# Kernel tuning notes

Hardware: AMD Instinct MI355X
Metric: run time of the kernel (lower is better)

## Reference

```python
import jax, jax.numpy as jnp
import numpy as np

N, XDIM, D, K = 400000, 128, 3, 4
TWO_PI = 2.0 * np.pi


def _scaled(k, shape):
    fan_in = shape[0]
    return jax.random.normal(k, shape, jnp.float32) * np.float32(1.0 / np.sqrt(fan_in))


def setup_inputs() -> dict:
    key = jax.random.key(0)
    ks = jax.random.split(key, 9)
    return {
        "x1": jax.random.normal(ks[0], (N, XDIM), jnp.float32),
        "enc_w1": _scaled(ks[1], (XDIM, 16)), "enc_b1": jnp.zeros((16,), jnp.float32),
        "enc_w2": _scaled(ks[2], (16, 8)),   "enc_b2": jnp.zeros((8,), jnp.float32),
        "enc_w3": _scaled(ks[3], (8, 1)),    "enc_b3": jnp.zeros((1,), jnp.float32),
        "dec_w1": _scaled(ks[4], (1, 8)),    "dec_b1": jnp.zeros((8,), jnp.float32),
        "dec_w2": _scaled(ks[5], (8, 16)),   "dec_b2": jnp.zeros((16,), jnp.float32),
        "dec_w3": _scaled(ks[6], (16, XDIM)),"dec_b3": jnp.zeros((XDIM,), jnp.float32),
        "est_w1": _scaled(ks[7], (D, 8)),    "est_b1": jnp.zeros((8,), jnp.float32),
        "est_w2": _scaled(ks[8], (8, K)),    "est_b2": jnp.zeros((K,), jnp.float32),
    }


def reference(x1, enc_w1, enc_b1, enc_w2, enc_b2, enc_w3, enc_b3,
              dec_w1, dec_b1, dec_w2, dec_b2, dec_w3, dec_b3,
              est_w1, est_b1, est_w2, est_b2):
    # encoder: Dense(16,tanh)->Dense(8,tanh)->Dense(1,tanh)
    h = jnp.tanh(x1 @ enc_w1 + enc_b1)
    h = jnp.tanh(h @ enc_w2 + enc_b2)
    z1 = jnp.tanh(h @ enc_w3 + enc_b3)            # [N,1]
    # decoder: Dense(8,tanh)->Dense(16,tanh)->Dense(xdim, linear)
    h = jnp.tanh(z1 @ dec_w1 + dec_b1)
    h = jnp.tanh(h @ dec_w2 + dec_b2)
    x2 = h @ dec_w3 + dec_b3                      # [N,xdim]

    # relative distances
    dist_cos = jnp.sum(x1 * x2, axis=1, keepdims=True) / (
        jnp.linalg.norm(x1, axis=1, keepdims=True) * jnp.linalg.norm(x2, axis=1, keepdims=True))
    dist_euc = jnp.linalg.norm(x1 - x2, axis=1, keepdims=True)
    z = jnp.concatenate([z1, dist_cos, dist_euc], axis=1)   # [N,D]

    # estimator: Dense(8,tanh)->Dense(K,softmax)
    gamma = jax.nn.softmax(jnp.tanh(z @ est_w1 + est_b1) @ est_w2 + est_b2)  # [N,K]

    # GMM parameters from soft assignments
    gamma_sum = jnp.sum(gamma, axis=0)                        # [K]
    phi = jnp.mean(gamma, axis=0)                             # [K]
    mu = jnp.einsum('ik,il->kl', gamma, z) / gamma_sum[:, None]          # [K,D]
    z_centered = jnp.sqrt(gamma)[:, :, None] * (z[:, None, :] - mu[None, :, :])  # [N,K,D]
    sigma = jnp.einsum('ikl,ikm->klm', z_centered, z_centered) / gamma_sum[:, None, None]  # [K,D,D]

    # per-sample energy
    z_mu = z[:, None, :] - mu[None, :, :]                     # [N,K,D]
    sigma_inv = jnp.linalg.inv(sigma)                         # [K,D,D]
    item1 = jnp.log(phi)[None, :]                             # [1,K]
    item2 = -0.5 * jnp.einsum('nkd,kde,nke->nk', z_mu, sigma_inv, z_mu)  # [N,K]
    sigma_det = jnp.linalg.det(TWO_PI * sigma)                # [K]
    item3 = jnp.log(jnp.sqrt(sigma_det))[None, :]             # [1,K]
    energy = -jnp.sum(item1 + item2 - item3, axis=1)          # [N]

    # loss
    lambda1, lambda2 = 0.01, 0.0001
    diag = jnp.diagonal(sigma, axis1=-2, axis2=-1)            # [K,D]
    loss3 = lambda2 * jnp.sum(1.0 / diag)
    loss2 = lambda1 * jnp.mean(energy)
    loss1 = jnp.mean(jnp.sum(jnp.square(x1 - x2), axis=1))
    loss = loss1 + loss2 + loss3
    return energy, loss
```

## Files before the change

### kernel.cpp

```cpp
#include <hip/hip_runtime.h>

#define NSAMP 400000
#define NBLK  1563


__device__ __forceinline__ float ftanh(float x) {
    float e = __expf(2.0f * x);
    return 1.0f - __fdividef(2.0f, e + 1.0f);
}

__global__ __launch_bounds__(256) void prep_kernel(const float* __restrict__ dw3,
                                                   const float* __restrict__ db3,
                                                   float* __restrict__ Gm,
                                                   float* __restrict__ gv,
                                                   float* __restrict__ bb) {
    int t = threadIdx.x;
    int a = t >> 4, b = t & 15;
    float s = 0.f;
    for (int j = 0; j < 128; ++j) s += dw3[a * 128 + j] * dw3[b * 128 + j];
    Gm[t] = s;
    if (t < 16) {
        float sg = 0.f;
        for (int j = 0; j < 128; ++j) sg += dw3[t * 128 + j] * db3[j];
        gv[t] = sg;
    }
    if (t == 0) {
        float sbv = 0.f;
        for (int j = 0; j < 128; ++j) sbv += db3[j] * db3[j];
        *bb = sbv;
    }
}

__global__ __launch_bounds__(256) void pass1_kernel(
    const float* __restrict__ x1,
    const float* __restrict__ ew1, const float* __restrict__ eb1,
    const float* __restrict__ ew2, const float* __restrict__ eb2,
    const float* __restrict__ ew3, const float* __restrict__ eb3,
    const float* __restrict__ dw1, const float* __restrict__ db1,
    const float* __restrict__ dw2, const float* __restrict__ db2,
    const float* __restrict__ dw3, const float* __restrict__ db3,
    const float* __restrict__ tw1, const float* __restrict__ tb1,
    const float* __restrict__ tw2, const float* __restrict__ tb2,
    const float* __restrict__ Gm, const float* __restrict__ gv,
    const float* __restrict__ bbp,
    double* __restrict__ acc, float4* __restrict__ zbuf) {
    int i = blockIdx.x * 256 + threadIdx.x;
    bool active = (i < NSAMP);
    int row = active ? i : 0;
    const float4* xr = (const float4*)(x1 + (size_t)row * 128);

    float u[16], v[16];
#pragma unroll
    for (int k = 0; k < 16; ++k) { u[k] = 0.f; v[k] = 0.f; }
    float s2 = 0.f, sb = 0.f;

    float4 buf[4];
#pragma unroll
    for (int c = 0; c < 4; ++c) buf[c] = xr[c];

#pragma unroll 1
    for (int blk = 0; blk < 8; ++blk) {
        float xe[16];
#pragma unroll
        for (int c = 0; c < 4; ++c) {
            xe[c * 4 + 0] = buf[c].x; xe[c * 4 + 1] = buf[c].y;
            xe[c * 4 + 2] = buf[c].z; xe[c * 4 + 3] = buf[c].w;
        }
        if (blk < 7) {
#pragma unroll
            for (int c = 0; c < 4; ++c) buf[c] = xr[(blk + 1) * 4 + c];
        }
        int j0 = blk * 16;
#pragma unroll
        for (int e = 0; e < 16; ++e) {
            float x = xe[e];
            s2 = fmaf(x, x, s2);
            sb = fmaf(x, db3[j0 + e], sb);
#pragma unroll
            for (int k = 0; k < 16; ++k) u[k] = fmaf(x, ew1[(j0 + e) * 16 + k], u[k]);
        }
#pragma unroll
        for (int q = 0; q < 16; ++q) {
            float a2 = v[q];
#pragma unroll
            for (int e = 0; e < 16; ++e) a2 = fmaf(xe[e], dw3[q * 128 + j0 + e], a2);
            v[q] = a2;
        }
    }

    float h1[16];
#pragma unroll
    for (int k = 0; k < 16; ++k) h1[k] = ftanh(u[k] + eb1[k]);
    float h2[8];
#pragma unroll
    for (int m = 0; m < 8; ++m) {
        float a2 = eb2[m];
#pragma unroll
        for (int k = 0; k < 16; ++k) a2 = fmaf(h1[k], ew2[k * 8 + m], a2);
        h2[m] = ftanh(a2);
    }
    float a3 = eb3[0];
#pragma unroll
    for (int m = 0; m < 8; ++m) a3 = fmaf(h2[m], ew3[m], a3);
    float z1 = ftanh(a3);

    float d1[8];
#pragma unroll
    for (int p = 0; p < 8; ++p) d1[p] = ftanh(fmaf(z1, dw1[p], db1[p]));
    float d2[16];
#pragma unroll
    for (int q = 0; q < 16; ++q) {
        float a2 = db2[q];
#pragma unroll
        for (int p = 0; p < 8; ++p) a2 = fmaf(d1[p], dw2[p * 16 + q], a2);
        d2[q] = ftanh(a2);
    }

    float dot = sb;
#pragma unroll
    for (int q = 0; q < 16; ++q) dot = fmaf(d2[q], v[q], dot);
    float n2 = *bbp;
#pragma unroll
    for (int a = 0; a < 16; ++a) {
        float ra = 2.0f * gv[a];
#pragma unroll
        for (int b = 0; b < 16; ++b) ra = fmaf(Gm[a * 16 + b], d2[b], ra);
        n2 = fmaf(d2[a], ra, n2);
    }
    n2 = fmaxf(n2, 1e-20f);
    float euc2 = fmaxf(s2 - 2.0f * dot + n2, 0.f);
    float deuc = sqrtf(euc2);
    float dcos = dot * rsqrtf(s2 * n2);

    float zf[3] = {z1, dcos, deuc};

    float e1[8];
#pragma unroll
    for (int p = 0; p < 8; ++p) {
        float a2 = tb1[p];
        a2 = fmaf(zf[0], tw1[0 * 8 + p], a2);
        a2 = fmaf(zf[1], tw1[1 * 8 + p], a2);
        a2 = fmaf(zf[2], tw1[2 * 8 + p], a2);
        e1[p] = ftanh(a2);
    }
    float lg[4];
#pragma unroll
    for (int k = 0; k < 4; ++k) {
        float a2 = tb2[k];
#pragma unroll
        for (int p = 0; p < 8; ++p) a2 = fmaf(e1[p], tw2[p * 4 + k], a2);
        lg[k] = a2;
    }
    float mx = fmaxf(fmaxf(lg[0], lg[1]), fmaxf(lg[2], lg[3]));
    float ex[4]; float se = 0.f;
#pragma unroll
    for (int k = 0; k < 4; ++k) { ex[k] = __expf(lg[k] - mx); se += ex[k]; }
    float inv = __fdividef(1.0f, se);
    float gam[4];
#pragma unroll
    for (int k = 0; k < 4; ++k) gam[k] = ex[k] * inv;

    if (active) zbuf[i] = make_float4(zf[0], zf[1], zf[2], 0.f);
    if (!active) { gam[0] = gam[1] = gam[2] = gam[3] = 0.f; euc2 = 0.f; }

    __shared__ float sPart[4][41];
    int lane = threadIdx.x & 63;
    int wid = threadIdx.x >> 6;

#define REDUCE_STORE(T, VAL) { float _v = (VAL);                          \
        _v += __shfl_down(_v, 32); _v += __shfl_down(_v, 16);             \
        _v += __shfl_down(_v, 8);  _v += __shfl_down(_v, 4);              \
        _v += __shfl_down(_v, 2);  _v += __shfl_down(_v, 1);              \
        if (lane == 0) sPart[wid][T] = _v; }

#pragma unroll
    for (int k = 0; k < 4; ++k) REDUCE_STORE(k, gam[k]);
#pragma unroll
    for (int k = 0; k < 4; ++k) {
#pragma unroll
        for (int d = 0; d < 3; ++d) REDUCE_STORE(4 + k * 3 + d, gam[k] * zf[d]);
    }
#pragma unroll
    for (int k = 0; k < 4; ++k) {
        REDUCE_STORE(16 + k * 6 + 0, gam[k] * zf[0] * zf[0]);
        REDUCE_STORE(16 + k * 6 + 1, gam[k] * zf[0] * zf[1]);
        REDUCE_STORE(16 + k * 6 + 2, gam[k] * zf[0] * zf[2]);
        REDUCE_STORE(16 + k * 6 + 3, gam[k] * zf[1] * zf[1]);
        REDUCE_STORE(16 + k * 6 + 4, gam[k] * zf[1] * zf[2]);
        REDUCE_STORE(16 + k * 6 + 5, gam[k] * zf[2] * zf[2]);
    }
    REDUCE_STORE(40, euc2);
#undef REDUCE_STORE

    __syncthreads();
    if (threadIdx.x < 41) {
        double s = (double)sPart[0][threadIdx.x] + (double)sPart[1][threadIdx.x]
                 + (double)sPart[2][threadIdx.x] + (double)sPart[3][threadIdx.x];
        unsafeAtomicAdd(&acc[threadIdx.x], s);
    }
}

__global__ void gmm_kernel(double* __restrict__ acc, float* __restrict__ P) {
    if (threadIdx.x != 0 || blockIdx.x != 0) return;
    double M[6] = {0, 0, 0, 0, 0, 0}, bv[3] = {0, 0, 0}, A = 0.0, loss3 = 0.0;
    const double TWO_PI = 6.283185307179586;
    for (int k = 0; k < 4; ++k) {
        double g = acc[k];
        double phi = g / (double)NSAMP;
        double mu0 = acc[4 + k * 3 + 0] / g;
        double mu1 = acc[4 + k * 3 + 1] / g;
        double mu2 = acc[4 + k * 3 + 2] / g;
        double S00 = acc[16 + k * 6 + 0] / g - mu0 * mu0;
        double S01 = acc[16 + k * 6 + 1] / g - mu0 * mu1;
        double S02 = acc[16 + k * 6 + 2] / g - mu0 * mu2;
        double S11 = acc[16 + k * 6 + 3] / g - mu1 * mu1;
        double S12 = acc[16 + k * 6 + 4] / g - mu1 * mu2;
        double S22 = acc[16 + k * 6 + 5] / g - mu2 * mu2;
        double c00 = S11 * S22 - S12 * S12;
        double c01 = S02 * S12 - S01 * S22;
        double c02 = S01 * S12 - S02 * S11;
        double det = S00 * c00 + S01 * c01 + S02 * c02;
        double id = 1.0 / det;
        double I00 = c00 * id, I01 = c01 * id, I02 = c02 * id;
        double I11 = (S00 * S22 - S02 * S02) * id;
        double I12 = (S01 * S02 - S00 * S12) * id;
        double I22 = (S00 * S11 - S01 * S01) * id;
        M[0] += I00; M[1] += I01; M[2] += I02; M[3] += I11; M[4] += I12; M[5] += I22;
        double b0 = I00 * mu0 + I01 * mu1 + I02 * mu2;
        double b1 = I01 * mu0 + I11 * mu1 + I12 * mu2;
        double b2 = I02 * mu0 + I12 * mu1 + I22 * mu2;
        bv[0] += b0; bv[1] += b1; bv[2] += b2;
        double quad = mu0 * b0 + mu1 * b1 + mu2 * b2;
        A += -log(phi) + 0.5 * log(TWO_PI * TWO_PI * TWO_PI * det) + 0.5 * quad;
        loss3 += 1e-4 * (1.0 / S00 + 1.0 / S11 + 1.0 / S22);
    }
    P[0] = (float)M[0]; P[1] = (float)M[1]; P[2] = (float)M[2];
    P[3] = (float)M[3]; P[4] = (float)M[4]; P[5] = (float)M[5];
    P[6] = (float)bv[0]; P[7] = (float)bv[1]; P[8] = (float)bv[2];
    P[9] = (float)A;
    acc[42] = acc[40] / (double)NSAMP + loss3;
}

__global__ __launch_bounds__(256) void energy_kernel(const float4* __restrict__ zbuf,
                                                     const float* __restrict__ P,
                                                     double* __restrict__ acc,
                                                     float* __restrict__ out) {
    int i = blockIdx.x * 256 + threadIdx.x;
    float e = 0.f;
    if (i < NSAMP) {
        float4 z4 = zbuf[i];
        float z0 = z4.x, z1 = z4.y, z2 = z4.z;
        float q = P[0] * z0 * z0 + P[3] * z1 * z1 + P[5] * z2 * z2
                + 2.f * (P[1] * z0 * z1 + P[2] * z0 * z2 + P[4] * z1 * z2);
        e = P[9] + 0.5f * q - (P[6] * z0 + P[7] * z1 + P[8] * z2);
        out[i] = e;
    }
    float s = e;
    s += __shfl_down(s, 32); s += __shfl_down(s, 16); s += __shfl_down(s, 8);
    s += __shfl_down(s, 4);  s += __shfl_down(s, 2);  s += __shfl_down(s, 1);
    __shared__ float sE[4];
    if ((threadIdx.x & 63) == 0) sE[threadIdx.x >> 6] = s;
    __syncthreads();
    if (threadIdx.x == 0) {
        double t = (double)sE[0] + (double)sE[1] + (double)sE[2] + (double)sE[3];
        unsafeAtomicAdd(&acc[41], t);
    }
}

__global__ void final_kernel(const double* __restrict__ acc, float* __restrict__ out) {
    if (threadIdx.x == 0 && blockIdx.x == 0)
        out[NSAMP] = (float)(acc[42] + 0.01 * acc[41] / (double)NSAMP);
}

extern "C" void kernel_launch(void* const* d_in, const int* in_sizes, int n_in,
                              void* d_out, int out_size, void* d_ws, size_t ws_size,
                              hipStream_t stream) {
    const float* x1  = (const float*)d_in[0];
    const float* ew1 = (const float*)d_in[1];
    const float* eb1 = (const float*)d_in[2];
    const float* ew2 = (const float*)d_in[3];
    const float* eb2 = (const float*)d_in[4];
    const float* ew3 = (const float*)d_in[5];
    const float* eb3 = (const float*)d_in[6];
    const float* dw1 = (const float*)d_in[7];
    const float* db1 = (const float*)d_in[8];
    const float* dw2 = (const float*)d_in[9];
    const float* db2 = (const float*)d_in[10];
    const float* dw3 = (const float*)d_in[11];
    const float* db3 = (const float*)d_in[12];
    const float* tw1 = (const float*)d_in[13];
    const float* tb1 = (const float*)d_in[14];
    const float* tw2 = (const float*)d_in[15];
    const float* tb2 = (const float*)d_in[16];
    float* out = (float*)d_out;
    char* ws = (char*)d_ws;
    double* acc = (double*)ws;
    float* P    = (float*)(ws + 384);
    float* Gm   = (float*)(ws + 1024);
    float* gv   = (float*)(ws + 2048);
    float* bb   = (float*)(ws + 2112);
    float4* zb  = (float4*)(ws + 4096);

    hipMemsetAsync(d_ws, 0, 512, stream);
    prep_kernel<<<1, 256, 0, stream>>>(dw3, db3, Gm, gv, bb);
    pass1_kernel<<<NBLK, 256, 0, stream>>>(x1, ew1, eb1, ew2, eb2, ew3, eb3,
                                           dw1, db1, dw2, db2, dw3, db3,
                                           tw1, tb1, tw2, tb2, Gm, gv, bb, acc, zb);
    gmm_kernel<<<1, 64, 0, stream>>>(acc, P);
    energy_kernel<<<NBLK, 256, 0, stream>>>(zb, P, acc, out);
    final_kernel<<<1, 64, 0, stream>>>(acc, out);
}
```

Before: 455.5 us.

## Stage x1 tiles via global_load_lds with swizzle, fold final kernel into energy

The main pass now loads each 16-column slice of x1 for the whole block cooperatively, using global_load_lds into a swizzled LDS buffer. This gives coalesced global reads in place of each thread streaming its own 512-byte row, and each thread then reads its row back from LDS. The cost is two block barriers per slice and the loss of the old register prefetch, so the load of the next slice no longer overlaps with compute. The final scalar kernel is removed: the last energy block, found with an atomic counter, writes the loss. The prep kernel also caches dw3 and db3 in shared memory.

```diff
diff --git a/kernel.cpp b/kernel.cpp
--- a/kernel.cpp
+++ b/kernel.cpp
@@ -14,19 +14,24 @@
                                                    float* __restrict__ Gm,
                                                    float* __restrict__ gv,
                                                    float* __restrict__ bb) {
+    __shared__ float sw3[2048];
+    __shared__ float sb3[128];
     int t = threadIdx.x;
+    for (int k = t; k < 2048; k += 256) sw3[k] = dw3[k];
+    if (t < 128) sb3[t] = db3[t];
+    __syncthreads();
     int a = t >> 4, b = t & 15;
     float s = 0.f;
-    for (int j = 0; j < 128; ++j) s += dw3[a * 128 + j] * dw3[b * 128 + j];
+    for (int j = 0; j < 128; ++j) s = fmaf(sw3[a * 128 + j], sw3[b * 128 + j], s);
     Gm[t] = s;
     if (t < 16) {
         float sg = 0.f;
-        for (int j = 0; j < 128; ++j) sg += dw3[t * 128 + j] * db3[j];
+        for (int j = 0; j < 128; ++j) sg = fmaf(sw3[t * 128 + j], sb3[j], sg);
         gv[t] = sg;
     }
     if (t == 0) {
         float sbv = 0.f;
-        for (int j = 0; j < 128; ++j) sbv += db3[j] * db3[j];
+        for (int j = 0; j < 128; ++j) sbv = fmaf(sb3[j], sb3[j], sbv);
         *bb = sbv;
     }
 }
@@ -44,31 +49,45 @@
     const float* __restrict__ Gm, const float* __restrict__ gv,
     const float* __restrict__ bbp,
     double* __restrict__ acc, float4* __restrict__ zbuf) {
-    int i = blockIdx.x * 256 + threadIdx.x;
+    __shared__ float4 lbuf[1024];
+    __shared__ float sPart[4][41];
+
+    int t = threadIdx.x;
+    int i = blockIdx.x * 256 + t;
     bool active = (i < NSAMP);
-    int row = active ? i : 0;
-    const float4* xr = (const float4*)(x1 + (size_t)row * 128);
+    int bbase = blockIdx.x * 256;
+    int w = t >> 6, lane = t & 63;
+    int sw2 = (t >> 1) & 3;
+    const float4* x1f4 = (const float4*)x1;
 
     float u[16], v[16];
 #pragma unroll
     for (int k = 0; k < 16; ++k) { u[k] = 0.f; v[k] = 0.f; }
     float s2 = 0.f, sb = 0.f;
 
-    float4 buf[4];
-#pragma unroll
-    for (int c = 0; c < 4; ++c) buf[c] = xr[c];
-
 #pragma unroll 1
     for (int blk = 0; blk < 8; ++blk) {
+#pragma unroll
+        for (int c2 = 0; c2 < 4; ++c2) {
+            int idx = (w * 4 + c2) * 64 + lane;
+            int row = idx >> 2, qs = idx & 3;
+            int q = qs ^ ((row >> 1) & 3);
+            int grow = bbase + row;
+            if (grow >= NSAMP) grow = NSAMP - 1;
+            const float4* src = x1f4 + (size_t)grow * 32 + blk * 4 + q;
+            float4* dst = lbuf + (w * 4 + c2) * 64;
+            __builtin_amdgcn_global_load_lds(
+                (const __attribute__((address_space(1))) void*)src,
+                (__attribute__((address_space(3))) void*)dst, 16, 0, 0);
+        }
+        __syncthreads();
+
         float xe[16];
 #pragma unroll
-        for (int c = 0; c < 4; ++c) {
-            xe[c * 4 + 0] = buf[c].x; xe[c * 4 + 1] = buf[c].y;
-            xe[c * 4 + 2] = buf[c].z; xe[c * 4 + 3] = buf[c].w;
-        }
-        if (blk < 7) {
-#pragma unroll
-            for (int c = 0; c < 4; ++c) buf[c] = xr[(blk + 1) * 4 + c];
+        for (int q = 0; q < 4; ++q) {
+            float4 w4 = lbuf[t * 4 + (q ^ sw2)];
+            xe[q * 4 + 0] = w4.x; xe[q * 4 + 1] = w4.y;
+            xe[q * 4 + 2] = w4.z; xe[q * 4 + 3] = w4.w;
         }
         int j0 = blk * 16;
 #pragma unroll
@@ -86,6 +105,7 @@
             for (int e = 0; e < 16; ++e) a2 = fmaf(xe[e], dw3[q * 128 + j0 + e], a2);
             v[q] = a2;
         }
+        __syncthreads();
     }
 
     float h1[16];
@@ -163,15 +183,14 @@
     if (active) zbuf[i] = make_float4(zf[0], zf[1], zf[2], 0.f);
     if (!active) { gam[0] = gam[1] = gam[2] = gam[3] = 0.f; euc2 = 0.f; }
 
-    __shared__ float sPart[4][41];
-    int lane = threadIdx.x & 63;
+    int rlane = threadIdx.x & 63;
     int wid = threadIdx.x >> 6;
 
 #define REDUCE_STORE(T, VAL) { float _v = (VAL);                          \
         _v += __shfl_down(_v, 32); _v += __shfl_down(_v, 16);             \
         _v += __shfl_down(_v, 8);  _v += __shfl_down(_v, 4);              \
         _v += __shfl_down(_v, 2);  _v += __shfl_down(_v, 1);              \
-        if (lane == 0) sPart[wid][T] = _v; }
+        if (rlane == 0) sPart[wid][T] = _v; }
 
 #pragma unroll
     for (int k = 0; k < 4; ++k) REDUCE_STORE(k, gam[k]);
@@ -244,6 +263,7 @@
 __global__ __launch_bounds__(256) void energy_kernel(const float4* __restrict__ zbuf,
                                                      const float* __restrict__ P,
                                                      double* __restrict__ acc,
+                                                     unsigned* __restrict__ cnt,
                                                      float* __restrict__ out) {
     int i = blockIdx.x * 256 + threadIdx.x;
     float e = 0.f;
@@ -264,12 +284,13 @@
     if (threadIdx.x == 0) {
         double t = (double)sE[0] + (double)sE[1] + (double)sE[2] + (double)sE[3];
         unsafeAtomicAdd(&acc[41], t);
-    }
-}
-
-__global__ void final_kernel(const double* __restrict__ acc, float* __restrict__ out) {
-    if (threadIdx.x == 0 && blockIdx.x == 0)
-        out[NSAMP] = (float)(acc[42] + 0.01 * acc[41] / (double)NSAMP);
+        __threadfence();
+        unsigned old = atomicAdd(cnt, 1u);
+        if (old == (unsigned)(NBLK - 1)) {
+            double tot = unsafeAtomicAdd(&acc[41], 0.0);
+            out[NSAMP] = (float)(acc[42] + 0.01 * tot / (double)NSAMP);
+        }
+    }
 }
 
 extern "C" void kernel_launch(void* const* d_in, const int* in_sizes, int n_in,
@@ -294,7 +315,8 @@
     const float* tb2 = (const float*)d_in[16];
     float* out = (float*)d_out;
     char* ws = (char*)d_ws;
-    double* acc = (double*)ws;
+    double* acc   = (double*)ws;
+    unsigned* cnt = (unsigned*)(ws + 352);
     float* P    = (float*)(ws + 384);
     float* Gm   = (float*)(ws + 1024);
     float* gv   = (float*)(ws + 2048);
@@ -307,6 +329,5 @@
                                            dw1, db1, dw2, db2, dw3, db3,
                                            tw1, tb1, tw2, tb2, Gm, gv, bb, acc, zb);
     gmm_kernel<<<1, 64, 0, stream>>>(acc, P);
-    energy_kernel<<<NBLK, 256, 0, stream>>>(zb, P, acc, out);
-    final_kernel<<<1, 64, 0, stream>>>(acc, out);
-}
+    energy_kernel<<<NBLK, 256, 0, stream>>>(zb, P, acc, cnt, out);
+}
```

New measurement: 472.9 us. +3.8%, slower.
